# Optimization experiments

Measured on AMD Instinct MI355X. Metric: run time of the kernel, lower is better.

Reference implementation:

```python
import jax, jax.numpy as jnp
import numpy as np

# regular 3x3 kernel grid: row 0 = dy, row 1 = dx, row-major over taps
REG = jnp.array([[-1, -1, -1, 0, 0, 0, 1, 1, 1],
                 [-1, 0, 1, -1, 0, 1, -1, 0, 1]], dtype=jnp.float32)
BN_EPS = 1e-5


def _conv3x3(x, w, b):
    y = jax.lax.conv_general_dilated(x, w, (1, 1), ((1, 1), (1, 1)),
                                     dimension_numbers=('NCHW', 'OIHW', 'NCHW'))
    return y + b[None, :, None, None]


def setup_inputs() -> dict:
    key = jax.random.key(0)
    ks = jax.random.split(key, 8)
    N, C, H, W = 8, 48, 96, 72
    s = 0.05  # small init so offsets stay local, like a trained net
    return {
        'x': jax.random.normal(ks[0], (N, C, H, W), jnp.float32),
        'tm_w': jax.random.normal(ks[1], (4, C, 3, 3), jnp.float32) * s,
        'tm_b': jax.random.normal(ks[2], (4,), jnp.float32) * s,
        'tr_w': jax.random.normal(ks[3], (2, C, 3, 3), jnp.float32) * s,
        'tr_b': jax.random.normal(ks[4], (2,), jnp.float32) * s,
        'mk_w': jax.random.normal(ks[5], (9, C, 3, 3), jnp.float32) * s,
        'mk_b': jnp.ones((9,), jnp.float32),
        'dw': jax.random.normal(ks[6], (C, C, 3, 3), jnp.float32) * s,
        'gamma': jnp.ones((C,), jnp.float32),
        'beta': jnp.zeros((C,), jnp.float32),
        'rmean': jnp.zeros((C,), jnp.float32),
        'rvar': jnp.ones((C,), jnp.float32),
    }


def reference(x, tm_w, tm_b, tr_w, tr_b, mk_w, mk_b, dw, gamma, beta, rmean, rvar):
    N, C, H, W = x.shape
    # per-pixel 2x2 transform matrix -> offsets = T @ REG - REG
    T = _conv3x3(x, tm_w, tm_b).transpose(0, 2, 3, 1).reshape(N, H, W, 2, 2)
    off = jnp.einsum('nhwij,jk->nhwik', T, REG) - REG          # [N,H,W,2,9]
    tr = _conv3x3(x, tr_w, tr_b)                               # [N,2,H,W]
    oy = off[..., 0, :] + tr[:, 0, :, :, None]                 # [N,H,W,9]
    ox = off[..., 1, :] + tr[:, 1, :, :, None]
    mask = _conv3x3(x, mk_w, mk_b).transpose(0, 2, 3, 1)       # [N,H,W,9]

    # sampling locations (stride=1, pad=1, dilation=1)
    ky = jnp.repeat(jnp.arange(3), 3).astype(x.dtype)          # tap row offsets 0..2
    kx = jnp.tile(jnp.arange(3), 3).astype(x.dtype)
    py = jnp.arange(H, dtype=x.dtype)[None, :, None, None] - 1.0 + ky + oy
    px = jnp.arange(W, dtype=x.dtype)[None, None, :, None] - 1.0 + kx + ox

    y0 = jnp.floor(py); x0 = jnp.floor(px)
    wy = (py - y0)[..., None]; wx = (px - x0)[..., None]
    y0i = y0.astype(jnp.int32); x0i = x0.astype(jnp.int32)
    nidx = jnp.arange(N)[:, None, None, None]

    def gather(yi, xi):
        valid = (yi >= 0) & (yi < H) & (xi >= 0) & (xi < W)
        v = x[nidx, :, jnp.clip(yi, 0, H - 1), jnp.clip(xi, 0, W - 1)]  # [N,H,W,9,C]
        return v * valid[..., None].astype(x.dtype)

    v00 = gather(y0i, x0i)
    v01 = gather(y0i, x0i + 1)
    v10 = gather(y0i + 1, x0i)
    v11 = gather(y0i + 1, x0i + 1)
    samp = (v00 * (1 - wy) * (1 - wx) + v01 * (1 - wy) * wx +
            v10 * wy * (1 - wx) + v11 * wy * wx)
    samp = samp * mask[..., None]                               # modulated (v2) mask

    out = jnp.einsum('nhwkc,ock->nohw', samp, dw.reshape(dw.shape[0], dw.shape[1], 9))
    # BatchNorm (eval mode, running stats) + residual + ReLU
    scale = (gamma / jnp.sqrt(rvar + BN_EPS))[None, :, None, None]
    out = (out - rmean[None, :, None, None]) * scale + beta[None, :, None, None]
    return jax.nn.relu(out + x)
```

## Files before the change

### kernel.cpp

```cpp
#include <hip/hip_runtime.h>
#include <math.h>
#include <stdint.h>

namespace {
constexpr int N = 8, C = 48, H = 96, W = 72;
constexpr int HW = H * W;
constexpr int P = N * HW;
constexpr float BN_EPS = 1e-5f;

constexpr int KSTEPS = 14;

constexpr int WS_ACONV = 0;
constexpr int ACONV_EL = KSTEPS * 64 * 8;
constexpr int WS_ADEF  = WS_ACONV + ACONV_EL * 2;
constexpr int ADEF_EL  = KSTEPS * 3 * 64 * 8;
constexpr int WS_SC    = WS_ADEF + ADEF_EL * 2;
constexpr int WS_BI    = WS_SC + 192;
constexpr int WS_XT    = 57728;

typedef __attribute__((ext_vector_type(8))) short     bf16x8;
typedef __attribute__((ext_vector_type(4))) float     f32x4;
typedef __attribute__((ext_vector_type(8))) _Float16  half8;
typedef __attribute__((ext_vector_type(4))) unsigned  u32x4;
typedef __attribute__((ext_vector_type(2))) unsigned  u32x2;
}

__device__ __forceinline__ unsigned short rne_bf16(float f) {
    unsigned u = __builtin_bit_cast(unsigned, f);
    return (unsigned short)((u + 0x7FFFu + ((u >> 16) & 1u)) >> 16);
}
__device__ __forceinline__ unsigned f2bf2(float a, float b) {
    unsigned ua = __builtin_bit_cast(unsigned, a);
    unsigned ub = __builtin_bit_cast(unsigned, b);
    return ((ua + 0x8000u) >> 16) | (((ub + 0x8000u) >> 16) << 16);
}

__global__ void prep_kernel(const float* __restrict__ tm_w, const float* __restrict__ tr_w,
                            const float* __restrict__ mk_w, const float* __restrict__ dw,
                            const float* __restrict__ gamma, const float* __restrict__ beta,
                            const float* __restrict__ rmean, const float* __restrict__ rvar,
                            unsigned char* __restrict__ wsb)
{
    int tid = blockIdx.x * blockDim.x + threadIdx.x;

    if (tid < ACONV_EL) {
        int i  = tid & 7;
        int l  = (tid >> 3) & 63;
        int ks = tid >> 9;
        int o  = l & 15;
        int Kg = ks * 32 + ((l >> 4) * 8) + i;
        int t  = Kg / 48, c = Kg % 48;
        float v = 0.f;
        if (o < 15 && t < 9) {
            if (o < 4)      v = tm_w[(o * C + c) * 9 + t];
            else if (o < 6) v = tr_w[((o - 4) * C + c) * 9 + t];
            else            v = mk_w[((o - 6) * C + c) * 9 + t];
        }
        ((unsigned short*)(wsb + WS_ACONV))[tid] = rne_bf16(v);
    }
    int t2 = tid - ACONV_EL;
    if (t2 >= 0 && t2 < ADEF_EL) {
        int i  = t2 & 7;
        int l  = (t2 >> 3) & 63;
        int r2 = t2 >> 9;
        int mt = r2 % 3;
        int ks = r2 / 3;
        int o  = mt * 16 + (l & 15);
        int Kg = ks * 32 + ((l >> 4) * 8) + i;
        int t  = Kg / 48, c = Kg % 48;
        float v = (t < 9) ? dw[(o * C + c) * 9 + t] : 0.f;
        ((unsigned short*)(wsb + WS_ADEF))[t2] = rne_bf16(v);
    }
    if (tid < C) {
        float sc = gamma[tid] * rsqrtf(rvar[tid] + BN_EPS);
        ((float*)(wsb + WS_SC))[tid] = sc;
        ((float*)(wsb + WS_BI))[tid] = beta[tid] - rmean[tid] * sc;
    }
}

__global__ __launch_bounds__(256) void transpose_kernel(
    const float* __restrict__ x, unsigned char* __restrict__ wsb)
{
    __shared__ float tile[48][64];
    int tid = threadIdx.x;
    int b   = blockIdx.x;
    int n   = b & 7;
    int hw0 = (b >> 3) * 64;

#pragma unroll
    for (int it = 0; it < 12; ++it) {
        int c = it * 4 + (tid >> 6);
        tile[c][tid & 63] = x[((size_t)(n * C + c)) * HW + hw0 + (tid & 63)];
    }
    __syncthreads();

    int px = tid >> 2;
    int cq = tid & 3;
    unsigned short* xt = (unsigned short*)(wsb + WS_XT);
    size_t base = ((size_t)(n * HW + hw0 + px)) * 48 + cq * 12;
    unsigned pk[6];
#pragma unroll
    for (int k = 0; k < 6; ++k) {
        _Float16 h0 = (_Float16)tile[cq * 12 + 2 * k][px];
        _Float16 h1 = (_Float16)tile[cq * 12 + 2 * k + 1][px];
        pk[k] = (unsigned)__builtin_bit_cast(unsigned short, h0) |
                ((unsigned)__builtin_bit_cast(unsigned short, h1) << 16);
    }
#pragma unroll
    for (int k = 0; k < 3; ++k)
        *(u32x2*)(xt + base + k * 4) = (u32x2){pk[2 * k], pk[2 * k + 1]};
}

__global__ __launch_bounds__(576, 5) void fused_kernel(
    const float* __restrict__ x,
    const float* __restrict__ tm_b, const float* __restrict__ tr_b,
    const float* __restrict__ mk_b,
    const unsigned char* __restrict__ wsb,
    float* __restrict__ out)
{
    __shared__ __align__(16) unsigned char lds[64 * 896 + 16 * 64 * 4];
    float* convout = (float*)(lds + 64 * 896);

    const int tid = threadIdx.x;
    const int l   = tid & 63;
    const int wv  = __builtin_amdgcn_readfirstlane(tid >> 6);

    const int b    = blockIdx.x;
    const int n    = b & 7;
    const int tile = b >> 3;
    const int hw   = tile * 64 + l;
    const int ph   = hw / W;
    const int pw   = hw - ph * W;

    const unsigned short* xtn = (const unsigned short*)(wsb + WS_XT) + (size_t)n * HW * 48;
    const int swz = (l & 7) << 4;
    const int rowbase = l * 896 + wv * 96;

    if (wv == 0) {
        *(u32x4*)(lds + ((l * 896 + 864) ^ swz)) = (u32x4){0u, 0u, 0u, 0u};
        *(u32x4*)(lds + ((l * 896 + 880) ^ swz)) = (u32x4){0u, 0u, 0u, 0u};
    }

    {
        int dy = wv / 3 - 1, dx = wv % 3 - 1;
        int hh = ph + dy, ww = pw + dx;
        bool v = ((unsigned)hh < (unsigned)H) && ((unsigned)ww < (unsigned)W);
        const unsigned short* src = xtn + (size_t)(v ? hh * W + ww : 0) * 48;
#pragma unroll
        for (int half = 0; half < 2; ++half) {
            half8 cv[3];
#pragma unroll
            for (int jc = 0; jc < 3; ++jc)
                cv[jc] = v ? *(const half8*)(src + half * 24 + jc * 8) : (half8)0;
#pragma unroll
            for (int jc = 0; jc < 3; ++jc) {
                u32x4 pk;
#pragma unroll
                for (int p = 0; p < 4; ++p)
                    pk[p] = f2bf2((float)cv[jc][2 * p], (float)cv[jc][2 * p + 1]);
                *(u32x4*)(lds + ((rowbase + half * 48 + jc * 16) ^ swz)) = pk;
            }
        }
    }
    __syncthreads();

    if (wv < 4) {
        const short* Ac = (const short*)(wsb + WS_ACONV);
        f32x4 cacc = {0.f, 0.f, 0.f, 0.f};
        int pxc = wv * 16 + (l & 15);
        int bbase = pxc * 896 + ((l >> 4) << 4);
#pragma unroll
        for (int ks = 0; ks < KSTEPS; ++ks) {
            bf16x8 bfr = *(const bf16x8*)(lds + ((bbase + ks * 64) ^ swz));
            bf16x8 afr = *(const bf16x8*)(Ac + (ks * 64 + l) * 8);
            cacc = __builtin_amdgcn_mfma_f32_16x16x32_bf16(afr, bfr, cacc, 0, 0, 0);
        }
        int rowg = (l >> 4) * 4;
#pragma unroll
        for (int r = 0; r < 4; ++r)
            convout[(rowg + r) * 64 + pxc] = cacc[r];
    }
    __syncthreads();

    float o_y, o_x, msk;
    {
        float T0 = convout[0 * 64 + l] + tm_b[0];
        float T1 = convout[1 * 64 + l] + tm_b[1];
        float T2 = convout[2 * 64 + l] + tm_b[2];
        float T3 = convout[3 * 64 + l] + tm_b[3];
        float R0 = convout[4 * 64 + l] + tr_b[0];
        float R1 = convout[5 * 64 + l] + tr_b[1];
        float ry = (float)(wv / 3) - 1.f;
        float rx = (float)(wv % 3) - 1.f;
        o_y = fmaf(T0, ry, fmaf(T1, rx, R0)) - ry;
        o_x = fmaf(T2, ry, fmaf(T3, rx, R1)) - rx;
        msk = convout[(6 + wv) * 64 + l] + mk_b[wv];
    }

    {
        float py  = (float)(ph + wv / 3 - 1) + o_y;
        float pxf = (float)(pw + wv % 3 - 1) + o_x;
        float y0f = floorf(py), x0f = floorf(pxf);
        float wy = py - y0f, wx = pxf - x0f;
        int y0 = (int)y0f, x0 = (int)x0f;
        int y1 = y0 + 1,  x1 = x0 + 1;
        bool vy0 = (unsigned)y0 < (unsigned)H;
        bool vy1 = (unsigned)y1 < (unsigned)H;
        bool vx0 = (unsigned)x0 < (unsigned)W;
        bool vx1 = (unsigned)x1 < (unsigned)W;
        int cy0 = min(max(y0, 0), H - 1) * W;
        int cy1 = min(max(y1, 0), H - 1) * W;
        int cx0 = min(max(x0, 0), W - 1);
        int cx1 = min(max(x1, 0), W - 1);
        float a00 = (vy0 && vx0) ? (1.f - wy) * (1.f - wx) * msk : 0.f;
        float a01 = (vy0 && vx1) ? (1.f - wy) * wx * msk         : 0.f;
        float a10 = (vy1 && vx0) ? wy * (1.f - wx) * msk         : 0.f;
        float a11 = (vy1 && vx1) ? wy * wx * msk                 : 0.f;
        const unsigned short* r00 = xtn + (size_t)(cy0 + cx0) * 48;
        const unsigned short* r01 = xtn + (size_t)(cy0 + cx1) * 48;
        const unsigned short* r10 = xtn + (size_t)(cy1 + cx0) * 48;
        const unsigned short* r11 = xtn + (size_t)(cy1 + cx1) * 48;

#pragma unroll
        for (int half = 0; half < 2; ++half) {
            half8 c00[3], c01[3], c10[3], c11[3];
#pragma unroll
            for (int jc = 0; jc < 3; ++jc) {
                c00[jc] = *(const half8*)(r00 + half * 24 + jc * 8);
                c01[jc] = *(const half8*)(r01 + half * 24 + jc * 8);
                c10[jc] = *(const half8*)(r10 + half * 24 + jc * 8);
                c11[jc] = *(const half8*)(r11 + half * 24 + jc * 8);
            }
#pragma unroll
            for (int jc = 0; jc < 3; ++jc) {
                u32x4 pk;
#pragma unroll
                for (int p = 0; p < 4; ++p) {
                    float e0 = (float)c00[jc][2 * p] * a00;
                    e0 = fmaf((float)c01[jc][2 * p], a01, e0);
                    e0 = fmaf((float)c10[jc][2 * p], a10, e0);
                    e0 = fmaf((float)c11[jc][2 * p], a11, e0);
                    float e1 = (float)c00[jc][2 * p + 1] * a00;
                    e1 = fmaf((float)c01[jc][2 * p + 1], a01, e1);
                    e1 = fmaf((float)c10[jc][2 * p + 1], a10, e1);
                    e1 = fmaf((float)c11[jc][2 * p + 1], a11, e1);
                    pk[p] = f2bf2(e0, e1);
                }
                *(u32x4*)(lds + ((rowbase + half * 48 + jc * 16) ^ swz)) = pk;
            }
        }
    }
    __syncthreads();

    const short* Ad = (const short*)(wsb + WS_ADEF);
    const float* sc = (const float*)(wsb + WS_SC);
    const float* bi = (const float*)(wsb + WS_BI);

#pragma unroll
    for (int rep = 0; rep < 2; ++rep) {
        int t = wv + rep * 9;
        if (t < 12) {
            int mt = t >> 2, nt = t & 3;
            int pxc = nt * 16 + (l & 15);
            int bbase = pxc * 896 + ((l >> 4) << 4);
            f32x4 acc = {0.f, 0.f, 0.f, 0.f};
#pragma unroll
            for (int ks = 0; ks < KSTEPS; ++ks) {
                bf16x8 bfr = *(const bf16x8*)(lds + ((bbase + ks * 64) ^ swz));
                bf16x8 afr = *(const bf16x8*)(Ad + ((ks * 3 + mt) * 64 + l) * 8);
                acc = __builtin_amdgcn_mfma_f32_16x16x32_bf16(afr, bfr, acc, 0, 0, 0);
            }
            int rowg = (l >> 4) * 4;
#pragma unroll
            for (int r = 0; r < 4; ++r) {
                int o = mt * 16 + rowg + r;
                size_t addr = ((size_t)(n * C + o)) * HW + tile * 64 + pxc;
                float v = fmaf(acc[r], sc[o], bi[o]) + x[addr];
                out[addr] = fmaxf(v, 0.f);
            }
        }
    }
}

extern "C" void kernel_launch(void* const* d_in, const int* in_sizes, int n_in,
                              void* d_out, int out_size, void* d_ws, size_t ws_size,
                              hipStream_t stream)
{
    const float* x     = (const float*)d_in[0];
    const float* tm_w  = (const float*)d_in[1];
    const float* tm_b  = (const float*)d_in[2];
    const float* tr_w  = (const float*)d_in[3];
    const float* tr_b  = (const float*)d_in[4];
    const float* mk_w  = (const float*)d_in[5];
    const float* mk_b  = (const float*)d_in[6];
    const float* dw    = (const float*)d_in[7];
    const float* gamma = (const float*)d_in[8];
    const float* beta  = (const float*)d_in[9];
    const float* rmean = (const float*)d_in[10];
    const float* rvar  = (const float*)d_in[11];
    float* out = (float*)d_out;
    unsigned char* wsb = (unsigned char*)d_ws;

    int prep_threads = ACONV_EL + ADEF_EL;
    hipLaunchKernelGGL(prep_kernel, dim3((prep_threads + 255) / 256), dim3(256), 0, stream,
                       tm_w, tr_w, mk_w, dw, gamma, beta, rmean, rvar, wsb);
    hipLaunchKernelGGL(transpose_kernel, dim3(P / 64), dim3(256), 0, stream, x, wsb);
    hipLaunchKernelGGL(fused_kernel, dim3(P / 64), dim3(576), 0, stream,
                       x, tm_b, tr_b, mk_b, wsb, out);
}
```

Before: 123.0 us.

## Switch to fp16 MFMA, 48-pixel tiles, and merge prep into transpose kernel

Merges the weight-prep kernel into the transpose kernel, which saves one launch. The MFMA operands move from bf16 to fp16 so the fp16 transposed input can be copied straight into LDS without conversion. Bilinear sampling now runs in packed fp16 arithmetic. Each block handles 48 pixels instead of 64, so the 9 waves map exactly onto a 3x3 grid of output tiles with no second pass. The risks are lower-precision fp16 accumulation in the sampling, partially idle lanes in the gather phase, and more blocks.

```diff
diff --git a/kernel.cpp b/kernel.cpp
--- a/kernel.cpp
+++ b/kernel.cpp
@@ -9,6 +9,7 @@
 constexpr float BN_EPS = 1e-5f;
 
 constexpr int KSTEPS = 14;
+constexpr int PXB    = 48;
 
 constexpr int WS_ACONV = 0;
 constexpr int ACONV_EL = KSTEPS * 64 * 8;
@@ -18,35 +19,56 @@
 constexpr int WS_BI    = WS_SC + 192;
 constexpr int WS_XT    = 57728;
 
-typedef __attribute__((ext_vector_type(8))) short     bf16x8;
+typedef __attribute__((ext_vector_type(8))) _Float16  half8;
 typedef __attribute__((ext_vector_type(4))) float     f32x4;
-typedef __attribute__((ext_vector_type(8))) _Float16  half8;
 typedef __attribute__((ext_vector_type(4))) unsigned  u32x4;
 typedef __attribute__((ext_vector_type(2))) unsigned  u32x2;
 }
 
-__device__ __forceinline__ unsigned short rne_bf16(float f) {
-    unsigned u = __builtin_bit_cast(unsigned, f);
-    return (unsigned short)((u + 0x7FFFu + ((u >> 16) & 1u)) >> 16);
-}
-__device__ __forceinline__ unsigned f2bf2(float a, float b) {
-    unsigned ua = __builtin_bit_cast(unsigned, a);
-    unsigned ub = __builtin_bit_cast(unsigned, b);
-    return ((ua + 0x8000u) >> 16) | (((ub + 0x8000u) >> 16) << 16);
-}
-
-__global__ void prep_kernel(const float* __restrict__ tm_w, const float* __restrict__ tr_w,
-                            const float* __restrict__ mk_w, const float* __restrict__ dw,
-                            const float* __restrict__ gamma, const float* __restrict__ beta,
-                            const float* __restrict__ rmean, const float* __restrict__ rvar,
-                            unsigned char* __restrict__ wsb)
+__global__ __launch_bounds__(256) void transpose_prep_kernel(
+    const float* __restrict__ x,
+    const float* __restrict__ tm_w, const float* __restrict__ tr_w,
+    const float* __restrict__ mk_w, const float* __restrict__ dw,
+    const float* __restrict__ gamma, const float* __restrict__ beta,
+    const float* __restrict__ rmean, const float* __restrict__ rvar,
+    unsigned char* __restrict__ wsb)
 {
-    int tid = blockIdx.x * blockDim.x + threadIdx.x;
-
-    if (tid < ACONV_EL) {
-        int i  = tid & 7;
-        int l  = (tid >> 3) & 63;
-        int ks = tid >> 9;
+    __shared__ float tile[48][64];
+    int tid = threadIdx.x;
+    int b   = blockIdx.x;
+    int n   = b & 7;
+    int hw0 = (b >> 3) * 64;
+
+#pragma unroll
+    for (int it = 0; it < 12; ++it) {
+        int c = it * 4 + (tid >> 6);
+        tile[c][tid & 63] = x[((size_t)(n * C + c)) * HW + hw0 + (tid & 63)];
+    }
+    __syncthreads();
+
+    {
+        int px = tid >> 2;
+        int cq = tid & 3;
+        unsigned short* xt = (unsigned short*)(wsb + WS_XT);
+        size_t base = ((size_t)(n * HW + hw0 + px)) * 48 + cq * 12;
+        unsigned pk[6];
+#pragma unroll
+        for (int k = 0; k < 6; ++k) {
+            _Float16 h0 = (_Float16)tile[cq * 12 + 2 * k][px];
+            _Float16 h1 = (_Float16)tile[cq * 12 + 2 * k + 1][px];
+            pk[k] = (unsigned)__builtin_bit_cast(unsigned short, h0) |
+                    ((unsigned)__builtin_bit_cast(unsigned short, h1) << 16);
+        }
+#pragma unroll
+        for (int k = 0; k < 3; ++k)
+            *(u32x2*)(xt + base + k * 4) = (u32x2){pk[2 * k], pk[2 * k + 1]};
+    }
+
+    int gtid = b * 256 + tid;
+    if (gtid < ACONV_EL) {
+        int i  = gtid & 7;
+        int l  = (gtid >> 3) & 63;
+        int ks = gtid >> 9;
         int o  = l & 15;
         int Kg = ks * 32 + ((l >> 4) * 8) + i;
         int t  = Kg / 48, c = Kg % 48;
@@ -56,9 +78,10 @@
             else if (o < 6) v = tr_w[((o - 4) * C + c) * 9 + t];
             else            v = mk_w[((o - 6) * C + c) * 9 + t];
         }
-        ((unsigned short*)(wsb + WS_ACONV))[tid] = rne_bf16(v);
-    }
-    int t2 = tid - ACONV_EL;
+        ((unsigned short*)(wsb + WS_ACONV))[gtid] =
+            __builtin_bit_cast(unsigned short, (_Float16)v);
+    }
+    int t2 = gtid - ACONV_EL;
     if (t2 >= 0 && t2 < ADEF_EL) {
         int i  = t2 & 7;
         int l  = (t2 >> 3) & 63;
@@ -69,46 +92,14 @@
         int Kg = ks * 32 + ((l >> 4) * 8) + i;
         int t  = Kg / 48, c = Kg % 48;
         float v = (t < 9) ? dw[(o * C + c) * 9 + t] : 0.f;
-        ((unsigned short*)(wsb + WS_ADEF))[t2] = rne_bf16(v);
-    }
-    if (tid < C) {
-        float sc = gamma[tid] * rsqrtf(rvar[tid] + BN_EPS);
-        ((float*)(wsb + WS_SC))[tid] = sc;
-        ((float*)(wsb + WS_BI))[tid] = beta[tid] - rmean[tid] * sc;
-    }
-}
-
-__global__ __launch_bounds__(256) void transpose_kernel(
-    const float* __restrict__ x, unsigned char* __restrict__ wsb)
-{
-    __shared__ float tile[48][64];
-    int tid = threadIdx.x;
-    int b   = blockIdx.x;
-    int n   = b & 7;
-    int hw0 = (b >> 3) * 64;
-
-#pragma unroll
-    for (int it = 0; it < 12; ++it) {
-        int c = it * 4 + (tid >> 6);
-        tile[c][tid & 63] = x[((size_t)(n * C + c)) * HW + hw0 + (tid & 63)];
-    }
-    __syncthreads();
-
-    int px = tid >> 2;
-    int cq = tid & 3;
-    unsigned short* xt = (unsigned short*)(wsb + WS_XT);
-    size_t base = ((size_t)(n * HW + hw0 + px)) * 48 + cq * 12;
-    unsigned pk[6];
-#pragma unroll
-    for (int k = 0; k < 6; ++k) {
-        _Float16 h0 = (_Float16)tile[cq * 12 + 2 * k][px];
-        _Float16 h1 = (_Float16)tile[cq * 12 + 2 * k + 1][px];
-        pk[k] = (unsigned)__builtin_bit_cast(unsigned short, h0) |
-                ((unsigned)__builtin_bit_cast(unsigned short, h1) << 16);
-    }
-#pragma unroll
-    for (int k = 0; k < 3; ++k)
-        *(u32x2*)(xt + base + k * 4) = (u32x2){pk[2 * k], pk[2 * k + 1]};
+        ((unsigned short*)(wsb + WS_ADEF))[t2] =
+            __builtin_bit_cast(unsigned short, (_Float16)v);
+    }
+    if (gtid < C) {
+        float sc = gamma[gtid] * rsqrtf(rvar[gtid] + BN_EPS);
+        ((float*)(wsb + WS_SC))[gtid] = sc;
+        ((float*)(wsb + WS_BI))[gtid] = beta[gtid] - rmean[gtid] * sc;
+    }
 }
 
 __global__ __launch_bounds__(576, 5) void fused_kernel(
@@ -118,8 +109,8 @@
     const unsigned char* __restrict__ wsb,
     float* __restrict__ out)
 {
-    __shared__ __align__(16) unsigned char lds[64 * 896 + 16 * 64 * 4];
-    float* convout = (float*)(lds + 64 * 896);
+    __shared__ __align__(16) unsigned char lds[PXB * 896 + 16 * PXB * 4];
+    float* convout = (float*)(lds + PXB * 896);
 
     const int tid = threadIdx.x;
     const int l   = tid & 63;
@@ -128,7 +119,7 @@
     const int b    = blockIdx.x;
     const int n    = b & 7;
     const int tile = b >> 3;
-    const int hw   = tile * 64 + l;
+    const int hw   = tile * PXB + (l < PXB ? l : PXB - 1);
     const int ph   = hw / W;
     const int pw   = hw - ph * W;
 
@@ -136,68 +127,55 @@
     const int swz = (l & 7) << 4;
     const int rowbase = l * 896 + wv * 96;
 
-    if (wv == 0) {
+    if (wv == 0 && l < PXB) {
         *(u32x4*)(lds + ((l * 896 + 864) ^ swz)) = (u32x4){0u, 0u, 0u, 0u};
         *(u32x4*)(lds + ((l * 896 + 880) ^ swz)) = (u32x4){0u, 0u, 0u, 0u};
     }
 
-    {
+    if (l < PXB) {
         int dy = wv / 3 - 1, dx = wv % 3 - 1;
         int hh = ph + dy, ww = pw + dx;
         bool v = ((unsigned)hh < (unsigned)H) && ((unsigned)ww < (unsigned)W);
-        const unsigned short* src = xtn + (size_t)(v ? hh * W + ww : 0) * 48;
-#pragma unroll
-        for (int half = 0; half < 2; ++half) {
-            half8 cv[3];
-#pragma unroll
-            for (int jc = 0; jc < 3; ++jc)
-                cv[jc] = v ? *(const half8*)(src + half * 24 + jc * 8) : (half8)0;
-#pragma unroll
-            for (int jc = 0; jc < 3; ++jc) {
-                u32x4 pk;
-#pragma unroll
-                for (int p = 0; p < 4; ++p)
-                    pk[p] = f2bf2((float)cv[jc][2 * p], (float)cv[jc][2 * p + 1]);
-                *(u32x4*)(lds + ((rowbase + half * 48 + jc * 16) ^ swz)) = pk;
-            }
-        }
-    }
-    __syncthreads();
-
-    if (wv < 4) {
-        const short* Ac = (const short*)(wsb + WS_ACONV);
+        const unsigned char* src = (const unsigned char*)(xtn + (size_t)(v ? hh * W + ww : 0) * 48);
+#pragma unroll
+        for (int j = 0; j < 6; ++j) {
+            u32x4 val = v ? *(const u32x4*)(src + j * 16) : (u32x4){0u, 0u, 0u, 0u};
+            *(u32x4*)(lds + ((rowbase + j * 16) ^ swz)) = val;
+        }
+    }
+    __syncthreads();
+
+    if (wv < 3) {
+        const _Float16* Ac = (const _Float16*)(wsb + WS_ACONV);
         f32x4 cacc = {0.f, 0.f, 0.f, 0.f};
         int pxc = wv * 16 + (l & 15);
         int bbase = pxc * 896 + ((l >> 4) << 4);
 #pragma unroll
         for (int ks = 0; ks < KSTEPS; ++ks) {
-            bf16x8 bfr = *(const bf16x8*)(lds + ((bbase + ks * 64) ^ swz));
-            bf16x8 afr = *(const bf16x8*)(Ac + (ks * 64 + l) * 8);
-            cacc = __builtin_amdgcn_mfma_f32_16x16x32_bf16(afr, bfr, cacc, 0, 0, 0);
+            half8 bfr = *(const half8*)(lds + ((bbase + ks * 64) ^ swz));
+            half8 afr = *(const half8*)(Ac + (ks * 64 + l) * 8);
+            cacc = __builtin_amdgcn_mfma_f32_16x16x32_f16(afr, bfr, cacc, 0, 0, 0);
         }
         int rowg = (l >> 4) * 4;
 #pragma unroll
         for (int r = 0; r < 4; ++r)
-            convout[(rowg + r) * 64 + pxc] = cacc[r];
-    }
-    __syncthreads();
-
-    float o_y, o_x, msk;
-    {
-        float T0 = convout[0 * 64 + l] + tm_b[0];
-        float T1 = convout[1 * 64 + l] + tm_b[1];
-        float T2 = convout[2 * 64 + l] + tm_b[2];
-        float T3 = convout[3 * 64 + l] + tm_b[3];
-        float R0 = convout[4 * 64 + l] + tr_b[0];
-        float R1 = convout[5 * 64 + l] + tr_b[1];
+            convout[(rowg + r) * PXB + pxc] = cacc[r];
+    }
+    __syncthreads();
+
+    if (l < PXB) {
+        float T0 = convout[0 * PXB + l] + tm_b[0];
+        float T1 = convout[1 * PXB + l] + tm_b[1];
+        float T2 = convout[2 * PXB + l] + tm_b[2];
+        float T3 = convout[3 * PXB + l] + tm_b[3];
+        float R0 = convout[4 * PXB + l] + tr_b[0];
+        float R1 = convout[5 * PXB + l] + tr_b[1];
         float ry = (float)(wv / 3) - 1.f;
         float rx = (float)(wv % 3) - 1.f;
-        o_y = fmaf(T0, ry, fmaf(T1, rx, R0)) - ry;
-        o_x = fmaf(T2, ry, fmaf(T3, rx, R1)) - rx;
-        msk = convout[(6 + wv) * 64 + l] + mk_b[wv];
-    }
-
-    {
+        float o_y = fmaf(T0, ry, fmaf(T1, rx, R0)) - ry;
+        float o_x = fmaf(T2, ry, fmaf(T3, rx, R1)) - rx;
+        float msk = convout[(6 + wv) * PXB + l] + mk_b[wv];
+
         float py  = (float)(ph + wv / 3 - 1) + o_y;
         float pxf = (float)(pw + wv % 3 - 1) + o_x;
         float y0f = floorf(py), x0f = floorf(pxf);
@@ -216,68 +194,58 @@
         float a01 = (vy0 && vx1) ? (1.f - wy) * wx * msk         : 0.f;
         float a10 = (vy1 && vx0) ? wy * (1.f - wx) * msk         : 0.f;
         float a11 = (vy1 && vx1) ? wy * wx * msk                 : 0.f;
-        const unsigned short* r00 = xtn + (size_t)(cy0 + cx0) * 48;
-        const unsigned short* r01 = xtn + (size_t)(cy0 + cx1) * 48;
-        const unsigned short* r10 = xtn + (size_t)(cy1 + cx0) * 48;
-        const unsigned short* r11 = xtn + (size_t)(cy1 + cx1) * 48;
-
-#pragma unroll
-        for (int half = 0; half < 2; ++half) {
+
+        _Float16 w00 = (_Float16)a00, w01 = (_Float16)a01;
+        _Float16 w10 = (_Float16)a10, w11 = (_Float16)a11;
+
+        const _Float16* r00 = (const _Float16*)(xtn + (size_t)(cy0 + cx0) * 48);
+        const _Float16* r01 = (const _Float16*)(xtn + (size_t)(cy0 + cx1) * 48);
+        const _Float16* r10 = (const _Float16*)(xtn + (size_t)(cy1 + cx0) * 48);
+        const _Float16* r11 = (const _Float16*)(xtn + (size_t)(cy1 + cx1) * 48);
+
+#pragma unroll
+        for (int ch = 0; ch < 2; ++ch) {
             half8 c00[3], c01[3], c10[3], c11[3];
 #pragma unroll
-            for (int jc = 0; jc < 3; ++jc) {
-                c00[jc] = *(const half8*)(r00 + half * 24 + jc * 8);
-                c01[jc] = *(const half8*)(r01 + half * 24 + jc * 8);
-                c10[jc] = *(const half8*)(r10 + half * 24 + jc * 8);
-                c11[jc] = *(const half8*)(r11 + half * 24 + jc * 8);
+            for (int j = 0; j < 3; ++j) {
+                int jj = ch * 3 + j;
+                c00[j] = *(const half8*)(r00 + jj * 8);
+                c01[j] = *(const half8*)(r01 + jj * 8);
+                c10[j] = *(const half8*)(r10 + jj * 8);
+                c11[j] = *(const half8*)(r11 + jj * 8);
             }
 #pragma unroll
-            for (int jc = 0; jc < 3; ++jc) {
-                u32x4 pk;
-#pragma unroll
-                for (int p = 0; p < 4; ++p) {
-                    float e0 = (float)c00[jc][2 * p] * a00;
-                    e0 = fmaf((float)c01[jc][2 * p], a01, e0);
-                    e0 = fmaf((float)c10[jc][2 * p], a10, e0);
-                    e0 = fmaf((float)c11[jc][2 * p], a11, e0);
-                    float e1 = (float)c00[jc][2 * p + 1] * a00;
-                    e1 = fmaf((float)c01[jc][2 * p + 1], a01, e1);
-                    e1 = fmaf((float)c10[jc][2 * p + 1], a10, e1);
-                    e1 = fmaf((float)c11[jc][2 * p + 1], a11, e1);
-                    pk[p] = f2bf2(e0, e1);
-                }
-                *(u32x4*)(lds + ((rowbase + half * 48 + jc * 16) ^ swz)) = pk;
+            for (int j = 0; j < 3; ++j) {
+                int jj = ch * 3 + j;
+                half8 s = c00[j] * w00 + c01[j] * w01 + c10[j] * w10 + c11[j] * w11;
+                *(u32x4*)(lds + ((rowbase + jj * 16) ^ swz)) = __builtin_bit_cast(u32x4, s);
             }
         }
     }
     __syncthreads();
 
-    const short* Ad = (const short*)(wsb + WS_ADEF);
-    const float* sc = (const float*)(wsb + WS_SC);
-    const float* bi = (const float*)(wsb + WS_BI);
-
-#pragma unroll
-    for (int rep = 0; rep < 2; ++rep) {
-        int t = wv + rep * 9;
-        if (t < 12) {
-            int mt = t >> 2, nt = t & 3;
-            int pxc = nt * 16 + (l & 15);
-            int bbase = pxc * 896 + ((l >> 4) << 4);
-            f32x4 acc = {0.f, 0.f, 0.f, 0.f};
-#pragma unroll
-            for (int ks = 0; ks < KSTEPS; ++ks) {
-                bf16x8 bfr = *(const bf16x8*)(lds + ((bbase + ks * 64) ^ swz));
-                bf16x8 afr = *(const bf16x8*)(Ad + ((ks * 3 + mt) * 64 + l) * 8);
-                acc = __builtin_amdgcn_mfma_f32_16x16x32_bf16(afr, bfr, acc, 0, 0, 0);
-            }
-            int rowg = (l >> 4) * 4;
-#pragma unroll
-            for (int r = 0; r < 4; ++r) {
-                int o = mt * 16 + rowg + r;
-                size_t addr = ((size_t)(n * C + o)) * HW + tile * 64 + pxc;
-                float v = fmaf(acc[r], sc[o], bi[o]) + x[addr];
-                out[addr] = fmaxf(v, 0.f);
-            }
+    {
+        const _Float16* Ad = (const _Float16*)(wsb + WS_ADEF);
+        const float* sc = (const float*)(wsb + WS_SC);
+        const float* bi = (const float*)(wsb + WS_BI);
+
+        int mt = wv / 3, nt = wv % 3;
+        int pxc = nt * 16 + (l & 15);
+        int bbase = pxc * 896 + ((l >> 4) << 4);
+        f32x4 acc = {0.f, 0.f, 0.f, 0.f};
+#pragma unroll
+        for (int ks = 0; ks < KSTEPS; ++ks) {
+            half8 bfr = *(const half8*)(lds + ((bbase + ks * 64) ^ swz));
+            half8 afr = *(const half8*)(Ad + ((ks * 3 + mt) * 64 + l) * 8);
+            acc = __builtin_amdgcn_mfma_f32_16x16x32_f16(afr, bfr, acc, 0, 0, 0);
+        }
+        int rowg = (l >> 4) * 4;
+#pragma unroll
+        for (int r = 0; r < 4; ++r) {
+            int o = mt * 16 + rowg + r;
+            size_t addr = ((size_t)(n * C + o)) * HW + tile * PXB + pxc;
+            float v = fmaf(acc[r], sc[o], bi[o]) + x[addr];
+            out[addr] = fmaxf(v, 0.f);
         }
     }
 }
@@ -301,10 +269,8 @@
     float* out = (float*)d_out;
     unsigned char* wsb = (unsigned char*)d_ws;
 
-    int prep_threads = ACONV_EL + ADEF_EL;
-    hipLaunchKernelGGL(prep_kernel, dim3((prep_threads + 255) / 256), dim3(256), 0, stream,
-                       tm_w, tr_w, mk_w, dw, gamma, beta, rmean, rvar, wsb);
-    hipLaunchKernelGGL(transpose_kernel, dim3(P / 64), dim3(256), 0, stream, x, wsb);
-    hipLaunchKernelGGL(fused_kernel, dim3(P / 64), dim3(576), 0, stream,
+    hipLaunchKernelGGL(transpose_prep_kernel, dim3(P / 64), dim3(256), 0, stream,
+                       x, tm_w, tr_w, mk_w, dw, gamma, beta, rmean, rvar, wsb);
+    hipLaunchKernelGGL(fused_kernel, dim3(P / PXB), dim3(576), 0, stream,
                        x, tm_b, tr_b, mk_b, wsb, out);
 }
```

After: 116.9 us. 1.05x faster.
